# Performance work log

Hardware: AMD Instinct MI355X
Metric: run time of the kernel (lower is better)

## Reference

```python
import jax, jax.numpy as jnp
import numpy as np

WL = 140        # window_length
TD_NUM = 14     # TimeDelayEnd - TimeDelaySta = 21 - 7
OFC = 119       # window_length - TimeDelayEnd
E1 = 119        # td_attn embed dim
E2 = 16         # cm_attn embed dim


def _mha(q, k, v, in_w, in_b, out_w, out_b):
    # single-head MultiheadAttention, torch convention: y = x @ W.T + b
    E = q.shape[-1]
    qp = q @ in_w[:E].T + in_b[:E]
    kp = k @ in_w[E:2 * E].T + in_b[E:2 * E]
    vp = v @ in_w[2 * E:].T + in_b[2 * E:]
    attn = jax.nn.softmax((qp * (E ** -0.5)) @ kp.T, axis=-1)
    return (attn @ vp) @ out_w.T + out_b


def setup_inputs() -> dict:
    key = jax.random.key(0)
    ks = jax.random.split(key, 24)
    n = lambda i, s: jax.random.normal(ks[i], s, dtype=jnp.float32) * 0.05
    return {
        "x": jax.random.normal(ks[0], (1, 1, 18, WL), dtype=jnp.float32),
        "td_in_w": n(1, (3 * E1, E1)), "td_in_b": n(2, (3 * E1,)),
        "td_out_w": n(3, (E1, E1)), "td_out_b": n(4, (E1,)),
        "cm_in_w": n(5, (4, 3 * E2, E2)), "cm_in_b": n(6, (4, 3 * E2)),
        "cm_out_w": n(7, (4, E2, E2)), "cm_out_b": n(8, (4, E2)),
        "mc_w": n(9, (2, 16)), "mc_b": n(10, (2,)),
        "max_fc_w": n(11, (16, 32)), "max_fc_b": n(12, (16,)),
        "proj_w": n(13, (2, 16)),
        "ln_g": jnp.ones((16,), jnp.float32), "ln_b": jnp.zeros((16,), jnp.float32),
        "fc_w": n(14, (2,)), "fc_b": n(15, (2,)),
        "out1_w": n(16, (OFC, 2 * OFC)), "out1_b": n(17, (OFC,)),
        "out2_w": n(18, (2, OFC)), "out2_b": n(19, (2,)),
    }


def reference(x, td_in_w, td_in_b, td_out_w, td_out_b,
              cm_in_w, cm_in_b, cm_out_w, cm_out_b,
              mc_w, mc_b, max_fc_w, max_fc_b, proj_w,
              ln_g, ln_b, fc_w, fc_b, out1_w, out1_b, out2_w, out2_b):
    wavA = x[0, 0, 0]            # [140]
    eeg = x[0, 0, 1:17]          # [16, 140]
    wavB = x[0, 0, 17]           # [140]

    # ChannelWav: vectorized sliding-window gather -> [OFC, TD_NUM]
    idx = jnp.arange(OFC)[:, None] + jnp.arange(TD_NUM)[None, :]
    wA_win = wavA[idx]           # [119, 14]
    wB_win = wavB[idx]

    eeg_q = eeg[:, WL - OFC:]    # [16, 119] (16 eeg channels as seq, embed=119)

    # time-delay attention: query=eeg (len 16), key/value=delayed wav (len 14)
    wA_att = _mha(eeg_q, wA_win.T, wA_win.T, td_in_w, td_in_b, td_out_w, td_out_b)  # [16,119]
    wB_att = _mha(eeg_q, wB_win.T, wB_win.T, td_in_w, td_in_b, td_out_w, td_out_b)

    # select_max: bmm + 1x1 conv + relu + fc + argmax over 16 scores
    vA = jax.nn.relu(mc_w[0] @ (eeg_q @ wA_att.T) + mc_b[0])   # [16]
    vB = jax.nn.relu(mc_w[1] @ (eeg_q @ wB_att.T) + mc_b[1])
    weight = jax.nn.relu(max_fc_w @ jnp.concatenate([vA, vB]) + max_fc_b)
    mi = jnp.argmax(weight)     # note: clamped into [0, TD_NUM) by jnp.take
    wA_sel = jnp.take(wA_win.T, mi, axis=0)   # [119]
    wB_sel = jnp.take(wB_win.T, mi, axis=0)

    # proj_audio: Conv1d(1,16,1,bias=False) == outer product with weight vector
    wA_p = proj_w[0][:, None] * wA_sel[None, :]   # [16,119]
    wB_p = proj_w[1][:, None] * wB_sel[None, :]

    # LayerNorm over the 16-channel axis
    et = eeg_q.T                                   # [119,16]
    mu = et.mean(-1, keepdims=True)
    var = et.var(-1, keepdims=True)
    eeg_ln = (((et - mu) / jnp.sqrt(var + 1e-5)) * ln_g + ln_b).T   # [16,119]

    data = [wA_p, eeg_ln, eeg_ln, wB_p]
    kv = [eeg_ln, wA_p, wB_p, eeg_ln]
    outs = [_mha(data[i].T, kv[i].T, kv[i].T,
                 cm_in_w[i], cm_in_b[i], cm_out_w[i], cm_out_b[i]).T
            for i in range(4)]                      # each [16,119]

    # tensordot + diag == per-position channel dot product
    d0 = jnp.einsum('ct,ct->t', outs[0], outs[1])   # [119]
    d1 = jnp.einsum('ct,ct->t', outs[3], outs[2])
    s0 = jax.nn.sigmoid(fc_w[0] * d0 + fc_b[0])
    s1 = jax.nn.sigmoid(fc_w[1] * d1 + fc_b[1])
    dd = jnp.concatenate([s0, s1])                  # [238]

    h = jax.nn.sigmoid(out1_w @ dd + out1_b)
    return jax.nn.sigmoid(out2_w @ h + out2_b)[None, :]   # [1,2]
```

## Files before the change

kernel.cpp:

```cpp
#include <hip/hip_runtime.h>
#include <math.h>


#define NWG 8
#define NT  1024

constexpr int WLEN = 140;
constexpr int TDN  = 14;
constexpr int NOFC = 119;

constexpr int G_V16 = 0;
constexpr int G_O   = 64;

constexpr int EEG = 0;
constexpr int WA  = 1904;
constexpr int WB  = 2044;
constexpr int LNT = 2184;
constexpr int QP4 = 4088;
constexpr int Z4  = 4564;
constexpr int UD  = 5040;
constexpr int WTT = 5160;
constexpr int WVV = 5280;
constexpr int VT  = 5400;
constexpr int SC4 = 5416;
constexpr int BKQ = 5472;
constexpr int CVB = 5476, CBO = 5477, MIX = 5478;
constexpr int WGT = 5480;
constexpr int WQK = 5500;
constexpr int WEV = 5516;
constexpr int AC  = 5532, BC = 5548;
constexpr int PKQ = 5568;
constexpr int VPS = 7472;
constexpr int S1O = 9852;
constexpr int S2O = 9971;
constexpr int OWS = 10090;
constexpr int OBS = 10346;
constexpr int DD  = 4088;
constexpr int HH  = 4328;
constexpr int ARENA = 10368;

struct Args {
  const float *x, *td_in_w, *td_in_b, *td_out_w, *td_out_b;
  const float *cm_in_w, *cm_in_b, *cm_out_w, *cm_out_b;
  const float *mc_w, *mc_b, *max_fc_w, *max_fc_b, *proj_w;
  const float *ln_g, *ln_b, *fc_w, *fc_b;
  const float *out1_w, *out1_b, *out2_w, *out2_b;
  float *out;
  unsigned int *bar;
  float *G;
};

__device__ __forceinline__ float sigmf(float v) {
  return 1.0f / (1.0f + __expf(-v));
}

__device__ __forceinline__ void gbar(unsigned int* p) {
  __syncthreads();
  if (threadIdx.x == 0) {
    __hip_atomic_fetch_add(p, 1u, __ATOMIC_ACQ_REL, __HIP_MEMORY_SCOPE_AGENT);
    while (__hip_atomic_load(p, __ATOMIC_RELAXED, __HIP_MEMORY_SCOPE_AGENT) < (unsigned)NWG) {
      __builtin_amdgcn_s_sleep(1);
    }
    __builtin_amdgcn_fence(__ATOMIC_ACQUIRE, "agent");
  }
  __syncthreads();
}

__device__ __forceinline__ float dot119(const float* __restrict__ w,
                                        const float* __restrict__ x,
                                        int lane16) {
  float a0 = 0.f, a1 = 0.f;
#pragma unroll
  for (int t = 0; t < 7; ++t) {
    float wv = w[lane16 + 16 * t];
    float xv = x[lane16 + 16 * t];
    if (t & 1) a1 += wv * xv; else a0 += wv * xv;
  }
  if (lane16 < 7) a0 += w[112 + lane16] * x[112 + lane16];
  float acc = a0 + a1;
#pragma unroll
  for (int m = 1; m < 16; m <<= 1) acc += __shfl_xor(acc, m);
  return acc;
}

__device__ __forceinline__ float dot16f4(const float* __restrict__ x,
                                         const float* __restrict__ w) {
  const float4* xa = (const float4*)x; const float4* wa = (const float4*)w;
  float4 x0 = xa[0], x1 = xa[1], x2 = xa[2], x3 = xa[3];
  float4 w0 = wa[0], w1 = wa[1], w2 = wa[2], w3 = wa[3];
  float d0 = x0.x*w0.x + x0.y*w0.y + x0.z*w0.z + x0.w*w0.w;
  float d1 = x1.x*w1.x + x1.y*w1.y + x1.z*w1.z + x1.w*w1.w;
  float d2 = x2.x*w2.x + x2.y*w2.y + x2.z*w2.z + x2.w*w2.w;
  float d3 = x3.x*w3.x + x3.y*w3.y + x3.z*w3.z + x3.w*w3.w;
  return (d0 + d1) + (d2 + d3);
}

__global__ __launch_bounds__(NT) void fused_cnn_kernel(Args a) {
  __shared__ __align__(16) float S[ARENA];
  const int tid = threadIdx.x;
  const int wgid = blockIdx.x;
  const int grp = tid >> 4;
  const int lane16 = tid & 15;
  float* G = a.G;

  const int s  = wgid >> 2;
  const int i0 = (wgid & 3) * 4;
  const int wavs = s ? WB : WA;
  const int m  = (wgid == 2) ? 1 : (wgid == 3) ? 2 : (wgid < 2 || wgid == 6) ? 0 : 3;
  const int r0 = (wgid == 1 || wgid == 5) ? 40 : (wgid >= 6) ? 80 : 0;
  const int nr = (wgid == 2 || wgid == 3) ? 119 : (wgid >= 6) ? 39 : 40;
  const bool heavy = (m == 0) || (m == 3);
  const int pr = (m >= 2) ? 1 : 0;
  const int wavm = (m <= 1) ? WA : WB;

  for (int t = tid; t < 16 * NOFC; t += NT) {
    int c = t / NOFC, tt = t - c * NOFC;
    S[EEG + t] = a.x[(1 + c) * WLEN + (WLEN - NOFC) + tt];
  }
  if (tid < WLEN) {
    S[WA + tid] = a.x[tid];
    S[WB + tid] = a.x[17 * WLEN + tid];
  }
  __syncthreads();

  for (int e = grp; e < NOFC; e += 64) {
    const float* wrow = a.td_in_w + e * NOFC;
    float w0 = wrow[lane16], w1 = wrow[lane16 + 16], w2 = wrow[lane16 + 32],
          w3 = wrow[lane16 + 48], w4 = wrow[lane16 + 64], w5 = wrow[lane16 + 80],
          w6 = wrow[lane16 + 96];
    float wt7 = (lane16 < 7) ? wrow[112 + lane16] : 0.0f;
    float b = a.td_in_b[e];
#pragma unroll
    for (int kk = 0; kk < 4; ++kk) {
      const float* x = S + EEG + (i0 + kk) * NOFC;
      float acc = w0 * x[lane16] + w1 * x[lane16 + 16] + w2 * x[lane16 + 32]
                + w3 * x[lane16 + 48] + w4 * x[lane16 + 64] + w5 * x[lane16 + 80]
                + w6 * x[lane16 + 96];
      if (lane16 < 7) acc += wt7 * x[112 + lane16];
#pragma unroll
      for (int mm = 1; mm < 16; mm <<= 1) acc += __shfl_xor(acc, mm);
      if (lane16 == 0) S[QP4 + kk * NOFC + e] = acc + b;
    }
  }
  __syncthreads();

  if (tid < NOFC) {
    float xv[16]; float mu = 0.f;
#pragma unroll
    for (int c = 0; c < 16; ++c) { xv[c] = S[EEG + c * NOFC + tid]; mu += xv[c]; }
    mu *= (1.0f / 16.0f);
    float var = 0.f;
#pragma unroll
    for (int c = 0; c < 16; ++c) { float d = xv[c] - mu; var += d * d; }
    var *= (1.0f / 16.0f);
    float inv = 1.0f / sqrtf(var + 1e-5f);
#pragma unroll
    for (int c = 0; c < 16; ++c)
      S[LNT + tid * 16 + c] = (xv[c] - mu) * inv * a.ln_g[c] + a.ln_b[c];
  }
  if (tid >= 128 && tid < 128 + NOFC) {
    int d = tid - 128;
    float acc = 0.f;
#pragma unroll
    for (int i = 0; i < 16; ++i) acc += a.mc_w[s * 16 + i] * S[EEG + i * NOFC + d];
    S[UD + d] = acc;
  }
  if (tid >= 256 && tid < 256 + NOFC) {
    int t = tid - 256;
    float a0 = 0.f, a1 = 0.f, a2 = 0.f, a3 = 0.f;
    for (int e = 0; e < NOFC; ++e) {
      float w = a.td_in_w[(NOFC + e) * NOFC + t];
      a0 += S[QP4 + e] * w;
      a1 += S[QP4 + NOFC + e] * w;
      a2 += S[QP4 + 2 * NOFC + e] * w;
      a3 += S[QP4 + 3 * NOFC + e] * w;
    }
    S[Z4 + t] = a0; S[Z4 + NOFC + t] = a1;
    S[Z4 + 2 * NOFC + t] = a2; S[Z4 + 3 * NOFC + t] = a3;
  }
  if (tid >= 384 && tid < 448) {
    int kk = (tid - 384) >> 4;
    float acc = dot119(S + QP4 + kk * NOFC, a.td_in_b + NOFC, lane16);
    if (lane16 == 0) S[BKQ + kk] = acc;
  }
  if (tid >= 512 && tid < 528) {
    int e = tid - 512;
    int row = heavy ? (m * 48 + e) : (m * 48 + 16 + e);
    float acc = 0.f;
#pragma unroll
    for (int c = 0; c < 16; ++c) acc += a.proj_w[pr * 16 + c] * a.cm_in_w[row * 16 + c];
    S[WQK + e] = acc;
  }
  if (!heavy && tid >= 528 && tid < 544) {
    int e = tid - 528;
    float acc = 0.f;
#pragma unroll
    for (int c = 0; c < 16; ++c) acc += a.proj_w[pr * 16 + c] * a.cm_in_w[(m * 48 + 32 + e) * 16 + c];
    S[WEV + e] = acc;
  }
  __syncthreads();

  if (tid < NOFC) {
    float acc = 0.f;
    for (int d = 0; d < NOFC; ++d) acc += S[UD + d] * a.td_out_w[d * NOFC + tid];
    S[WTT + tid] = acc;
  } else if (heavy) {
    for (int o = tid - 128; o < 4080; o += 896) {
      if (o < 1904) {
        int u = o >> 4, e = o & 15;
        S[PKQ + u * 16 + e] = dot16f4(S + LNT + u * 16, a.cm_in_w + (m * 48 + 16 + e) * 16)
                              + a.cm_in_b[m * 48 + 16 + e];
      } else if (o < 3808) {
        int o2 = o - 1904, u = o2 >> 4, e = o2 & 15;
        S[VPS + u * 20 + e] = dot16f4(S + LNT + u * 16, a.cm_in_w + (m * 48 + 32 + e) * 16)
                              + a.cm_in_b[m * 48 + 32 + e];
      } else if (o < 4064) {
        int o2 = o - 3808, c = o2 >> 4, e = o2 & 15;
        S[OWS + e * 16 + c] = a.cm_out_w[m * 256 + o2];
      } else {
        S[OBS + o - 4064] = a.cm_out_b[m * 16 + (o - 4064)];
      }
    }
  } else {
    for (int o = tid - 128; o < 1904; o += 896) {
      int t = o >> 4, e = o & 15;
      S[PKQ + t * 16 + e] = dot16f4(S + LNT + t * 16, a.cm_in_w + (m * 48 + e) * 16)
                            + a.cm_in_b[m * 48 + e];
    }
  }
  __syncthreads();

  if (tid < NOFC) {
    float acc = 0.f;
    for (int e = 0; e < NOFC; ++e) acc += S[WTT + e] * a.td_in_w[(2 * NOFC + e) * NOFC + tid];
    S[WVV + tid] = acc;
  }
  if (grp >= 8 && grp < 64) {
    int idx = grp - 8;
    if (idx < 56) {
      int kk = idx / TDN, j = idx - kk * TDN;
      float acc = dot119(S + wavs + j, S + Z4 + kk * NOFC, lane16);
      if (lane16 == 0)
        S[SC4 + kk * TDN + j] = 0.09166984970282113f * (acc + S[BKQ + kk]);
    }
  }
  __syncthreads();

  if (tid < 4) {
    float* r = S + SC4 + tid * TDN;
    float mx = r[0];
#pragma unroll
    for (int j = 1; j < TDN; ++j) mx = fmaxf(mx, r[j]);
    float sum = 0.f;
#pragma unroll
    for (int j = 0; j < TDN; ++j) { float p = __expf(r[j] - mx); r[j] = p; sum += p; }
    float inv = 1.0f / sum;
#pragma unroll
    for (int j = 0; j < TDN; ++j) r[j] *= inv;
  }
  if (grp >= 1 && grp < 15) {
    int j = grp - 1;
    float acc = dot119(S + wavs + j, S + WVV, lane16);
    if (lane16 == 0) S[VT + j] = acc;
  }
  if (grp == 15) {
    float acc = dot119(a.td_in_b + 2 * NOFC, S + WTT, lane16);
    if (lane16 == 0) S[CVB] = acc;
  }
  if (grp == 16) {
    float acc = dot119(S + UD, a.td_out_b, lane16);
    if (lane16 == 0) S[CBO] = acc;
  }
  if (tid >= 288) {
    if (heavy) {
      int idx = tid - 288;
      if (idx < 238) {
        int u = (idx < NOFC) ? idx : idx - NOFC;
        const float* kpr = S + PKQ + u * 16;
        float acc = 0.f;
        if (idx < NOFC) {
#pragma unroll
          for (int e = 0; e < 16; ++e) acc += S[WQK + e] * kpr[e];
          S[S1O + u] = acc;
        } else {
#pragma unroll
          for (int e = 0; e < 16; ++e) acc += a.cm_in_b[m * 48 + e] * kpr[e];
          S[S2O + u] = acc;
        }
      }
    } else {
      int idx = tid - 288;
      if (idx < NOFC) {
        float acc = 0.f;
#pragma unroll
        for (int e = 0; e < 16; ++e) acc += S[PKQ + idx * 16 + e] * S[WQK + e];
        S[S1O + idx] = acc;
      } else if (idx >= 128 && idx < 144) {
        int c = idx - 128;
        float a1 = 0.f, b1 = 0.f;
#pragma unroll
        for (int e = 0; e < 16; ++e) {
          float ow = a.cm_out_w[m * 256 + c * 16 + e];
          a1 += ow * S[WEV + e];
          b1 += ow * a.cm_in_b[m * 48 + 32 + e];
        }
        S[AC + c] = a1;
        S[BC + c] = b1 + a.cm_out_b[m * 16 + c];
      }
    }
  }
  __syncthreads();

  if (tid < 4) {
    float acc = 0.f;
#pragma unroll
    for (int j = 0; j < TDN; ++j) acc += S[SC4 + tid * TDN + j] * S[VT + j];
    float v = acc + S[CVB] + S[CBO] + a.mc_b[s];
    G[G_V16 + s * 16 + i0 + tid] = fmaxf(v, 0.f);
  }
  gbar(a.bar + 0);

  if (tid < 16) {
    float acc = a.max_fc_b[tid];
#pragma unroll
    for (int c = 0; c < 32; ++c) acc += a.max_fc_w[tid * 32 + c] * G[G_V16 + c];
    S[WGT + tid] = fmaxf(acc, 0.f);
  }
  __syncthreads();
  if (tid == 0) {
    float best = S[WGT]; int mi = 0;
    for (int r = 1; r < 16; ++r) {
      float w = S[WGT + r];
      if (w > best) { best = w; mi = r; }
    }
    if (mi > TDN - 1) mi = TDN - 1;
    S[MIX] = (float)mi;
  }
  __syncthreads();

  {
    const int mi = (int)S[MIX];
    if (heavy) {
      if (grp < nr) {
        const int t = r0 + grp;
        const float wsel = S[wavm + t + mi];
        float p[8];
        float mx = -1e30f;
#pragma unroll
        for (int cc = 0; cc < 8; ++cc) {
          int u = lane16 + cc * 16;
          float sc = (u < NOFC) ? 0.25f * (wsel * S[S1O + u] + S[S2O + u]) : -1e30f;
          p[cc] = sc;
          mx = fmaxf(mx, sc);
        }
#pragma unroll
        for (int d = 1; d < 16; d <<= 1) mx = fmaxf(mx, __shfl_xor(mx, d));
        float sum = 0.f;
#pragma unroll
        for (int cc = 0; cc < 8; ++cc) { p[cc] = __expf(p[cc] - mx); sum += p[cc]; }
#pragma unroll
        for (int d = 1; d < 16; d <<= 1) sum += __shfl_xor(sum, d);
        float inv = 1.0f / sum;

        float oa[16];
#pragma unroll
        for (int e = 0; e < 16; ++e) oa[e] = 0.f;
#pragma unroll
        for (int cc = 0; cc < 8; ++cc) {
          int u = lane16 + cc * 16;
          if (u < NOFC) {
            const float4* v4 = (const float4*)(S + VPS + u * 20);
            float4 v0 = v4[0], v1 = v4[1], v2 = v4[2], v3 = v4[3];
            float pv = p[cc];
            oa[0] += pv*v0.x; oa[1] += pv*v0.y; oa[2] += pv*v0.z; oa[3] += pv*v0.w;
            oa[4] += pv*v1.x; oa[5] += pv*v1.y; oa[6] += pv*v1.z; oa[7] += pv*v1.w;
            oa[8] += pv*v2.x; oa[9] += pv*v2.y; oa[10] += pv*v2.z; oa[11] += pv*v2.w;
            oa[12] += pv*v3.x; oa[13] += pv*v3.y; oa[14] += pv*v3.z; oa[15] += pv*v3.w;
          }
        }
#pragma unroll
        for (int e = 0; e < 16; ++e) {
#pragma unroll
          for (int d = 1; d < 16; d <<= 1) oa[e] += __shfl_xor(oa[e], d);
          oa[e] *= inv;
        }
        float accp = S[OBS + lane16];
#pragma unroll
        for (int e = 0; e < 16; ++e) accp += oa[e] * S[OWS + e * 16 + lane16];
        G[G_O + (m * NOFC + t) * 16 + lane16] = accp;
      }
    } else {
      for (int r = grp; r < NOFC; r += 64) {
        const float gt = S[S1O + r];
        float s0 = 0.f, s1a = 0.f;
#pragma unroll
        for (int cc = 0; cc < 8; ++cc) {
          int u = lane16 + cc * 16;
          if (u < NOFC) {
            float w = S[wavm + u + mi];
            float e1 = __expf(0.25f * gt * w);
            s0 += e1; s1a += e1 * w;
          }
        }
#pragma unroll
        for (int d = 1; d < 16; d <<= 1) {
          s0 += __shfl_xor(s0, d);
          s1a += __shfl_xor(s1a, d);
        }
        float h = s1a / s0;
        G[G_O + (m * NOFC + r) * 16 + lane16] = h * S[AC + lane16] + S[BC + lane16];
      }
    }
  }
  gbar(a.bar + 16);

  if (wgid == 0) {
    for (int o = tid; o < 2 * NOFC; o += NT) {
      int half = o / NOFC, t = o - half * NOFC;
      const float* A = G + G_O + ((half ? 3 : 0) * NOFC + t) * 16;
      const float* B = G + G_O + ((half ? 2 : 1) * NOFC + t) * 16;
      float acc = 0.f;
#pragma unroll
      for (int c = 0; c < 16; ++c) acc += A[c] * B[c];
      S[DD + o] = sigmf(a.fc_w[half] * acc + a.fc_b[half]);
    }
    __syncthreads();
    for (int o = grp; o < NOFC; o += 64) {
      const float* wrow = a.out1_w + o * 238;
      float a0 = 0.f, a1 = 0.f;
#pragma unroll
      for (int t = 0; t < 14; ++t) {
        float wv = wrow[lane16 + 16 * t];
        float xv = S[DD + lane16 + 16 * t];
        if (t & 1) a1 += wv * xv; else a0 += wv * xv;
      }
      if (lane16 < 14) a0 += wrow[224 + lane16] * S[DD + 224 + lane16];
      float acc = a0 + a1;
#pragma unroll
      for (int mm = 1; mm < 16; mm <<= 1) acc += __shfl_xor(acc, mm);
      if (lane16 == 0) S[HH + o] = sigmf(acc + a.out1_b[o]);
    }
    __syncthreads();
    if (tid < 32) {
      int o2 = tid >> 4;
      const float* wrow = a.out2_w + o2 * NOFC;
      float a0 = 0.f;
#pragma unroll
      for (int t = 0; t < 8; ++t) {
        int idx = lane16 + 16 * t;
        if (idx < NOFC) a0 += wrow[idx] * S[HH + idx];
      }
      float acc = a0;
#pragma unroll
      for (int mm = 1; mm < 16; mm <<= 1) acc += __shfl_xor(acc, mm);
      if (lane16 == 0) a.out[o2] = sigmf(acc + a.out2_b[o2]);
    }
  }
}

extern "C" void kernel_launch(void* const* d_in, const int* in_sizes, int n_in,
                              void* d_out, int out_size, void* d_ws, size_t ws_size,
                              hipStream_t stream) {
  Args a;
  a.x        = (const float*)d_in[0];
  a.td_in_w  = (const float*)d_in[1];
  a.td_in_b  = (const float*)d_in[2];
  a.td_out_w = (const float*)d_in[3];
  a.td_out_b = (const float*)d_in[4];
  a.cm_in_w  = (const float*)d_in[5];
  a.cm_in_b  = (const float*)d_in[6];
  a.cm_out_w = (const float*)d_in[7];
  a.cm_out_b = (const float*)d_in[8];
  a.mc_w     = (const float*)d_in[9];
  a.mc_b     = (const float*)d_in[10];
  a.max_fc_w = (const float*)d_in[11];
  a.max_fc_b = (const float*)d_in[12];
  a.proj_w   = (const float*)d_in[13];
  a.ln_g     = (const float*)d_in[14];
  a.ln_b     = (const float*)d_in[15];
  a.fc_w     = (const float*)d_in[16];
  a.fc_b     = (const float*)d_in[17];
  a.out1_w   = (const float*)d_in[18];
  a.out1_b   = (const float*)d_in[19];
  a.out2_w   = (const float*)d_in[20];
  a.out2_b   = (const float*)d_in[21];
  a.out      = (float*)d_out;
  a.bar      = (unsigned int*)d_ws;
  a.G        = (float*)((char*)d_ws + 512);

  hipMemsetAsync(d_ws, 0, 512, stream);
  fused_cnn_kernel<<<dim3(NWG), dim3(NT), 0, stream>>>(a);
}
```

Before: 36.05 us.

## Repartition cross-modal attention per stream and distribute output MLP across workgroups

Each workgroup now owns one stream (A or B) and a 30-row slice, computing the heavy attention and the folded light attention together so that the per-position dot product and sigmoid happen locally. Only the 238 gating values go through global memory instead of four 119x16 output tensors. The final out1/out2 MLP is split across all 8 workgroups, with out1 rows prefetched into LDS, and finished with atomic accumulation plus a last-arriver completion counter. This replaces the serial single-workgroup tail. Several barrier phases are merged, argmax becomes a wave shuffle reduction, and the max-subtraction in softmax is dropped, which risks overflow. The atomic accumulators in the barrier buffer also need to be zeroed before every launch.

```diff
diff --git a/kernel.cpp b/kernel.cpp
--- a/kernel.cpp
+++ b/kernel.cpp
@@ -10,7 +10,7 @@
 constexpr int NOFC = 119;
 
 constexpr int G_V16 = 0;
-constexpr int G_O   = 64;
+constexpr int G_DD  = 64;
 
 constexpr int EEG = 0;
 constexpr int WA  = 1904;
@@ -24,20 +24,33 @@
 constexpr int VT  = 5400;
 constexpr int SC4 = 5416;
 constexpr int BKQ = 5472;
-constexpr int CVB = 5476, CBO = 5477, MIX = 5478;
-constexpr int WGT = 5480;
-constexpr int WQK = 5500;
-constexpr int WEV = 5516;
-constexpr int AC  = 5532, BC = 5548;
-constexpr int PKQ = 5568;
-constexpr int VPS = 7472;
-constexpr int S1O = 9852;
-constexpr int S2O = 9971;
-constexpr int OWS = 10090;
-constexpr int OBS = 10346;
-constexpr int DD  = 4088;
-constexpr int HH  = 4328;
-constexpr int ARENA = 10368;
+constexpr int CVB = 5476, CBO = 5477;
+constexpr int WQH = 5480;
+constexpr int WKL = 5496;
+constexpr int WVL = 5512;
+constexpr int WQT = 5528;
+constexpr int CST = 5544;
+constexpr int AC  = 5548;
+constexpr int BC  = 5564;
+constexpr int G1L = 5580;
+constexpr int MXT = 5612;
+constexpr int MXB = 6124;
+constexpr int KPH = 6144;
+constexpr int VPS = 8048;
+constexpr int S1H = 10428;
+constexpr int S2H = 10547;
+constexpr int OWS = 10668;
+constexpr int OBS = 10924;
+constexpr int O1W = 10944;
+constexpr int O1B = 14544;
+constexpr int O2WS= 14560;
+constexpr int O2B = 14590;
+constexpr int FCW = 14592;
+constexpr int FCB = 14594;
+constexpr int DDL = 14596;
+constexpr int HHL = 14836;
+constexpr int VSL = 14852;
+constexpr int ARENA = 14884;
 
 struct Args {
   const float *x, *td_in_w, *td_in_b, *td_out_w, *td_out_b;
@@ -105,13 +118,12 @@
 
   const int s  = wgid >> 2;
   const int i0 = (wgid & 3) * 4;
-  const int wavs = s ? WB : WA;
-  const int m  = (wgid == 2) ? 1 : (wgid == 3) ? 2 : (wgid < 2 || wgid == 6) ? 0 : 3;
-  const int r0 = (wgid == 1 || wgid == 5) ? 40 : (wgid >= 6) ? 80 : 0;
-  const int nr = (wgid == 2 || wgid == 3) ? 119 : (wgid >= 6) ? 39 : 40;
-  const bool heavy = (m == 0) || (m == 3);
-  const int pr = (m >= 2) ? 1 : 0;
-  const int wavm = (m <= 1) ? WA : WB;
+  const int mh = s ? 3 : 0;
+  const int lm = s ? 2 : 1;
+  const int q4 = wgid & 3;
+  const int r0 = q4 * 30;
+  const int nr = (q4 == 3) ? 29 : 30;
+  const int wavX = s ? WB : WA;
 
   for (int t = tid; t < 16 * NOFC; t += NT) {
     int c = t / NOFC, tt = t - c * NOFC;
@@ -120,6 +132,30 @@
   if (tid < WLEN) {
     S[WA + tid] = a.x[tid];
     S[WB + tid] = a.x[17 * WLEN + tid];
+  }
+  if (tid < 512) {
+    int t16 = tid >> 5, c32 = tid & 31;
+    S[MXT + c32 * 16 + t16] = a.max_fc_w[tid];
+  }
+  if (tid < 16)  S[MXB + tid] = a.max_fc_b[tid];
+  for (int idx = tid; idx < 15 * 238; idx += NT) {
+    int rl = idx / 238, c = idx - rl * 238;
+    int r = wgid * 15 + rl;
+    S[O1W + rl * 240 + c] = (r < NOFC) ? a.out1_w[r * 238 + c] : 0.0f;
+  }
+  if (tid < 15) {
+    int r = wgid * 15 + tid;
+    S[O1B + tid] = (r < NOFC) ? a.out1_b[r] : 0.0f;
+  }
+  if (tid < 30) {
+    int o = tid / 15, j = tid - o * 15;
+    int r = wgid * 15 + j;
+    S[O2WS + tid] = (r < NOFC) ? a.out2_w[o * NOFC + r] : 0.0f;
+  }
+  if (tid < 2) {
+    S[O2B + tid] = a.out2_b[tid];
+    S[FCW + tid] = a.fc_w[tid];
+    S[FCB + tid] = a.fc_b[tid];
   }
   __syncthreads();
 
@@ -142,6 +178,15 @@
       if (lane16 == 0) S[QP4 + kk * NOFC + e] = acc + b;
     }
   }
+  if (grp >= 55) {
+    int d = (grp - 55) * 16 + lane16;
+    if (d < NOFC) {
+      float acc = 0.f;
+#pragma unroll
+      for (int i = 0; i < 16; ++i) acc += a.mc_w[s * 16 + i] * S[EEG + i * NOFC + d];
+      S[UD + d] = acc;
+    }
+  }
   __syncthreads();
 
   if (tid < NOFC) {
@@ -157,16 +202,8 @@
 #pragma unroll
     for (int c = 0; c < 16; ++c)
       S[LNT + tid * 16 + c] = (xv[c] - mu) * inv * a.ln_g[c] + a.ln_b[c];
-  }
-  if (tid >= 128 && tid < 128 + NOFC) {
-    int d = tid - 128;
-    float acc = 0.f;
-#pragma unroll
-    for (int i = 0; i < 16; ++i) acc += a.mc_w[s * 16 + i] * S[EEG + i * NOFC + d];
-    S[UD + d] = acc;
-  }
-  if (tid >= 256 && tid < 256 + NOFC) {
-    int t = tid - 256;
+  } else if (tid >= 128 && tid < 128 + NOFC) {
+    int t = tid - 128;
     float a0 = 0.f, a1 = 0.f, a2 = 0.f, a3 = 0.f;
     for (int e = 0; e < NOFC; ++e) {
       float w = a.td_in_w[(NOFC + e) * NOFC + t];
@@ -177,136 +214,143 @@
     }
     S[Z4 + t] = a0; S[Z4 + NOFC + t] = a1;
     S[Z4 + 2 * NOFC + t] = a2; S[Z4 + 3 * NOFC + t] = a3;
-  }
-  if (tid >= 384 && tid < 448) {
-    int kk = (tid - 384) >> 4;
+  } else if (tid >= 256 && tid < 320) {
+    int kk = (tid - 256) >> 4;
     float acc = dot119(S + QP4 + kk * NOFC, a.td_in_b + NOFC, lane16);
     if (lane16 == 0) S[BKQ + kk] = acc;
-  }
-  if (tid >= 512 && tid < 528) {
-    int e = tid - 512;
-    int row = heavy ? (m * 48 + e) : (m * 48 + 16 + e);
-    float acc = 0.f;
-#pragma unroll
-    for (int c = 0; c < 16; ++c) acc += a.proj_w[pr * 16 + c] * a.cm_in_w[row * 16 + c];
-    S[WQK + e] = acc;
-  }
-  if (!heavy && tid >= 528 && tid < 544) {
-    int e = tid - 528;
-    float acc = 0.f;
-#pragma unroll
-    for (int c = 0; c < 16; ++c) acc += a.proj_w[pr * 16 + c] * a.cm_in_w[(m * 48 + 32 + e) * 16 + c];
-    S[WEV + e] = acc;
+  } else if (tid >= 320 && tid < 320 + NOFC) {
+    int t = tid - 320;
+    float acc = 0.f;
+    for (int d = 0; d < NOFC; ++d) acc += S[UD + d] * a.td_out_w[d * NOFC + t];
+    S[WTT + t] = acc;
+  } else if (tid >= 448 && tid < 464) {
+    int e = tid - 448;
+    float acc = 0.f;
+#pragma unroll
+    for (int c = 0; c < 16; ++c) acc += a.proj_w[s * 16 + c] * a.cm_in_w[(mh * 48 + e) * 16 + c];
+    S[WQH + e] = acc;
+  } else if (tid >= 464 && tid < 480) {
+    int e = tid - 464;
+    float acc = 0.f;
+#pragma unroll
+    for (int c = 0; c < 16; ++c) acc += a.proj_w[s * 16 + c] * a.cm_in_w[(lm * 48 + 16 + e) * 16 + c];
+    S[WKL + e] = acc;
+  } else if (tid >= 480 && tid < 496) {
+    int e = tid - 480;
+    float acc = 0.f;
+#pragma unroll
+    for (int c = 0; c < 16; ++c) acc += a.proj_w[s * 16 + c] * a.cm_in_w[(lm * 48 + 32 + e) * 16 + c];
+    S[WVL + e] = acc;
+  }
+  if (grp >= 36) {
+#pragma unroll
+    for (int rnd = 0; rnd < 2; ++rnd) {
+      int idx = (grp - 36) + rnd * 28;
+      if (idx < 56) {
+        int kk = idx / TDN, j = idx - kk * TDN;
+        float acc = dot119(S + wavX + j, S + Z4 + kk * NOFC, lane16);
+        if (lane16 == 0)
+          S[SC4 + kk * TDN + j] = 0.09166984970282113f * (acc + S[BKQ + kk]);
+      }
+    }
   }
   __syncthreads();
 
   if (tid < NOFC) {
     float acc = 0.f;
-    for (int d = 0; d < NOFC; ++d) acc += S[UD + d] * a.td_out_w[d * NOFC + tid];
-    S[WTT + tid] = acc;
-  } else if (heavy) {
-    for (int o = tid - 128; o < 4080; o += 896) {
+    for (int e = 0; e < NOFC; ++e) acc += S[WTT + e] * a.td_in_w[(2 * NOFC + e) * NOFC + tid];
+    S[WVV + tid] = acc;
+  } else if (tid >= 120 && tid < 124) {
+    int k = tid - 120;
+    float* r = S + SC4 + k * TDN;
+    float mx = r[0];
+#pragma unroll
+    for (int j = 1; j < TDN; ++j) mx = fmaxf(mx, r[j]);
+    float sum = 0.f;
+#pragma unroll
+    for (int j = 0; j < TDN; ++j) { float p = __expf(r[j] - mx); r[j] = p; sum += p; }
+    float inv = 1.0f / sum;
+#pragma unroll
+    for (int j = 0; j < TDN; ++j) r[j] *= inv;
+  } else if (tid >= 128 && tid < 144) {
+    int c = tid - 128;
+    float acc = 0.f;
+#pragma unroll
+    for (int e = 0; e < 16; ++e) acc += a.cm_in_w[(lm * 48 + e) * 16 + c] * S[WKL + e];
+    S[WQT + c] = acc;
+  } else if (tid == 144) {
+    float acc = 0.f;
+#pragma unroll
+    for (int e = 0; e < 16; ++e) acc += a.cm_in_b[lm * 48 + e] * S[WKL + e];
+    S[CST] = acc;
+  } else if (tid >= 160 && tid < 176) {
+    int c = tid - 160;
+    float acc = 0.f;
+#pragma unroll
+    for (int e = 0; e < 16; ++e) acc += a.cm_out_w[lm * 256 + c * 16 + e] * S[WVL + e];
+    S[AC + c] = acc;
+  } else if (tid >= 176 && tid < 192) {
+    int c = tid - 176;
+    float acc = 0.f;
+#pragma unroll
+    for (int e = 0; e < 16; ++e) acc += a.cm_out_w[lm * 256 + c * 16 + e] * a.cm_in_b[lm * 48 + 32 + e];
+    S[BC + c] = acc + a.cm_out_b[lm * 16 + c];
+  } else if (tid == 192) {
+    float acc = 0.f;
+    for (int e = 0; e < NOFC; ++e) acc += a.td_in_b[2 * NOFC + e] * S[WTT + e];
+    S[CVB] = acc;
+  } else if (tid == 193) {
+    float acc = 0.f;
+    for (int d = 0; d < NOFC; ++d) acc += S[UD + d] * a.td_out_b[d];
+    S[CBO] = acc;
+  }
+  if (tid >= 256) {
+    for (int o = tid - 256; o < 4080; o += 768) {
       if (o < 1904) {
         int u = o >> 4, e = o & 15;
-        S[PKQ + u * 16 + e] = dot16f4(S + LNT + u * 16, a.cm_in_w + (m * 48 + 16 + e) * 16)
-                              + a.cm_in_b[m * 48 + 16 + e];
+        S[KPH + o] = dot16f4(S + LNT + u * 16, a.cm_in_w + (mh * 48 + 16 + e) * 16)
+                     + a.cm_in_b[mh * 48 + 16 + e];
       } else if (o < 3808) {
         int o2 = o - 1904, u = o2 >> 4, e = o2 & 15;
-        S[VPS + u * 20 + e] = dot16f4(S + LNT + u * 16, a.cm_in_w + (m * 48 + 32 + e) * 16)
-                              + a.cm_in_b[m * 48 + 32 + e];
+        S[VPS + u * 20 + e] = dot16f4(S + LNT + u * 16, a.cm_in_w + (mh * 48 + 32 + e) * 16)
+                              + a.cm_in_b[mh * 48 + 32 + e];
       } else if (o < 4064) {
         int o2 = o - 3808, c = o2 >> 4, e = o2 & 15;
-        S[OWS + e * 16 + c] = a.cm_out_w[m * 256 + o2];
+        S[OWS + e * 16 + c] = a.cm_out_w[mh * 256 + o2];
       } else {
-        S[OBS + o - 4064] = a.cm_out_b[m * 16 + (o - 4064)];
+        S[OBS + o - 4064] = a.cm_out_b[mh * 16 + (o - 4064)];
       }
     }
-  } else {
-    for (int o = tid - 128; o < 1904; o += 896) {
-      int t = o >> 4, e = o & 15;
-      S[PKQ + t * 16 + e] = dot16f4(S + LNT + t * 16, a.cm_in_w + (m * 48 + e) * 16)
-                            + a.cm_in_b[m * 48 + e];
-    }
-  }
-  __syncthreads();
-
-  if (tid < NOFC) {
-    float acc = 0.f;
-    for (int e = 0; e < NOFC; ++e) acc += S[WTT + e] * a.td_in_w[(2 * NOFC + e) * NOFC + tid];
-    S[WVV + tid] = acc;
-  }
-  if (grp >= 8 && grp < 64) {
-    int idx = grp - 8;
-    if (idx < 56) {
-      int kk = idx / TDN, j = idx - kk * TDN;
-      float acc = dot119(S + wavs + j, S + Z4 + kk * NOFC, lane16);
-      if (lane16 == 0)
-        S[SC4 + kk * TDN + j] = 0.09166984970282113f * (acc + S[BKQ + kk]);
-    }
-  }
-  __syncthreads();
-
-  if (tid < 4) {
-    float* r = S + SC4 + tid * TDN;
-    float mx = r[0];
-#pragma unroll
-    for (int j = 1; j < TDN; ++j) mx = fmaxf(mx, r[j]);
-    float sum = 0.f;
-#pragma unroll
-    for (int j = 0; j < TDN; ++j) { float p = __expf(r[j] - mx); r[j] = p; sum += p; }
-    float inv = 1.0f / sum;
-#pragma unroll
-    for (int j = 0; j < TDN; ++j) r[j] *= inv;
-  }
-  if (grp >= 1 && grp < 15) {
-    int j = grp - 1;
-    float acc = dot119(S + wavs + j, S + WVV, lane16);
-    if (lane16 == 0) S[VT + j] = acc;
-  }
-  if (grp == 15) {
-    float acc = dot119(a.td_in_b + 2 * NOFC, S + WTT, lane16);
-    if (lane16 == 0) S[CVB] = acc;
-  }
-  if (grp == 16) {
-    float acc = dot119(S + UD, a.td_out_b, lane16);
-    if (lane16 == 0) S[CBO] = acc;
-  }
-  if (tid >= 288) {
-    if (heavy) {
-      int idx = tid - 288;
-      if (idx < 238) {
-        int u = (idx < NOFC) ? idx : idx - NOFC;
-        const float* kpr = S + PKQ + u * 16;
-        float acc = 0.f;
-        if (idx < NOFC) {
-#pragma unroll
-          for (int e = 0; e < 16; ++e) acc += S[WQK + e] * kpr[e];
-          S[S1O + u] = acc;
-        } else {
-#pragma unroll
-          for (int e = 0; e < 16; ++e) acc += a.cm_in_b[m * 48 + e] * kpr[e];
-          S[S2O + u] = acc;
-        }
-      }
+  }
+  __syncthreads();
+
+  if (grp < TDN) {
+    float acc = dot119(S + wavX + grp, S + WVV, lane16);
+    if (lane16 == 0) S[VT + grp] = acc;
+  }
+  if (tid >= 256 && tid < 256 + 30) {
+    int rl = tid - 256;
+    if (rl < nr) {
+      int t = r0 + rl;
+      float acc = S[CST];
+#pragma unroll
+      for (int c = 0; c < 16; ++c) acc += S[LNT + t * 16 + c] * S[WQT + c];
+      S[G1L + rl] = acc;
+    }
+  }
+  if (tid >= 512 && tid < 512 + 238) {
+    int idx = tid - 512;
+    int u = (idx < NOFC) ? idx : idx - NOFC;
+    const float* kpr = S + KPH + u * 16;
+    float acc = 0.f;
+    if (idx < NOFC) {
+#pragma unroll
+      for (int e = 0; e < 16; ++e) acc += S[WQH + e] * kpr[e];
+      S[S1H + u] = acc;
     } else {
-      int idx = tid - 288;
-      if (idx < NOFC) {
-        float acc = 0.f;
-#pragma unroll
-        for (int e = 0; e < 16; ++e) acc += S[PKQ + idx * 16 + e] * S[WQK + e];
-        S[S1O + idx] = acc;
-      } else if (idx >= 128 && idx < 144) {
-        int c = idx - 128;
-        float a1 = 0.f, b1 = 0.f;
-#pragma unroll
-        for (int e = 0; e < 16; ++e) {
-          float ow = a.cm_out_w[m * 256 + c * 16 + e];
-          a1 += ow * S[WEV + e];
-          b1 += ow * a.cm_in_b[m * 48 + 32 + e];
-        }
-        S[AC + c] = a1;
-        S[BC + c] = b1 + a.cm_out_b[m * 16 + c];
-      }
+#pragma unroll
+      for (int e = 0; e < 16; ++e) acc += a.cm_in_b[mh * 48 + e] * kpr[e];
+      S[S2H + u] = acc;
     }
   }
   __syncthreads();
@@ -320,140 +364,129 @@
   }
   gbar(a.bar + 0);
 
-  if (tid < 16) {
-    float acc = a.max_fc_b[tid];
-#pragma unroll
-    for (int c = 0; c < 32; ++c) acc += a.max_fc_w[tid * 32 + c] * G[G_V16 + c];
-    S[WGT + tid] = fmaxf(acc, 0.f);
+  if (tid < 32) S[VSL + tid] = G[G_V16 + tid];
+  __syncthreads();
+  int mi;
+  {
+    float wl = S[MXB + lane16];
+#pragma unroll
+    for (int c = 0; c < 32; ++c) wl += S[MXT + c * 16 + lane16] * S[VSL + c];
+    wl = fmaxf(wl, 0.f);
+    float mx = wl;
+#pragma unroll
+    for (int d = 1; d < 16; d <<= 1) mx = fmaxf(mx, __shfl_xor(mx, d));
+    int cand = (wl == mx) ? lane16 : 99;
+#pragma unroll
+    for (int d = 1; d < 16; d <<= 1) cand = min(cand, __shfl_xor(cand, d));
+    mi = min(cand, TDN - 1);
+  }
+
+  if (grp < nr) {
+    const int t = r0 + grp;
+    const float wselq = S[wavX + t + mi];
+    float p[8];
+    float sum = 0.f;
+#pragma unroll
+    for (int cc = 0; cc < 8; ++cc) {
+      int u = lane16 + cc * 16;
+      float e1 = 0.f;
+      if (u < NOFC)
+        e1 = __expf(0.25f * (wselq * S[S1H + u] + S[S2H + u]));
+      p[cc] = e1;
+      sum += e1;
+    }
+#pragma unroll
+    for (int d = 1; d < 16; d <<= 1) sum += __shfl_xor(sum, d);
+    float inv = 1.0f / sum;
+
+    float oa[16];
+#pragma unroll
+    for (int e = 0; e < 16; ++e) oa[e] = 0.f;
+#pragma unroll
+    for (int cc = 0; cc < 8; ++cc) {
+      int u = lane16 + cc * 16;
+      if (u < NOFC) {
+        const float4* v4 = (const float4*)(S + VPS + u * 20);
+        float4 v0 = v4[0], v1 = v4[1], v2 = v4[2], v3 = v4[3];
+        float pv = p[cc];
+        oa[0] += pv*v0.x; oa[1] += pv*v0.y; oa[2] += pv*v0.z; oa[3] += pv*v0.w;
+        oa[4] += pv*v1.x; oa[5] += pv*v1.y; oa[6] += pv*v1.z; oa[7] += pv*v1.w;
+        oa[8] += pv*v2.x; oa[9] += pv*v2.y; oa[10] += pv*v2.z; oa[11] += pv*v2.w;
+        oa[12] += pv*v3.x; oa[13] += pv*v3.y; oa[14] += pv*v3.z; oa[15] += pv*v3.w;
+      }
+    }
+#pragma unroll
+    for (int e = 0; e < 16; ++e) {
+#pragma unroll
+      for (int d = 1; d < 16; d <<= 1) oa[e] += __shfl_xor(oa[e], d);
+    }
+    float oc = S[OBS + lane16];
+#pragma unroll
+    for (int e = 0; e < 16; ++e) oc += oa[e] * inv * S[OWS + e * 16 + lane16];
+    float dA = oc * S[AC + lane16];
+    float dB = oc * S[BC + lane16];
+#pragma unroll
+    for (int d = 1; d < 16; d <<= 1) {
+      dA += __shfl_xor(dA, d);
+      dB += __shfl_xor(dB, d);
+    }
+    const float g = S[G1L + grp];
+    float s0 = 0.f, s1a = 0.f;
+#pragma unroll
+    for (int cc = 0; cc < 8; ++cc) {
+      int u = lane16 + cc * 16;
+      if (u < NOFC) {
+        float w = S[wavX + u + mi];
+        float e1 = __expf(0.25f * g * w);
+        s0 += e1; s1a += e1 * w;
+      }
+    }
+#pragma unroll
+    for (int d = 1; d < 16; d <<= 1) {
+      s0 += __shfl_xor(s0, d);
+      s1a += __shfl_xor(s1a, d);
+    }
+    float h = s1a / s0;
+    float dval = h * dA + dB;
+    if (lane16 == 0)
+      G[G_DD + s * NOFC + t] = sigmf(S[FCW + s] * dval + S[FCB + s]);
+  }
+  gbar(a.bar + 16);
+
+  if (tid < 238) S[DDL + tid] = G[G_DD + tid];
+  __syncthreads();
+  if (grp < 15) {
+    int r = wgid * 15 + grp;
+    float acc = 0.f;
+#pragma unroll
+    for (int k = 0; k < 15; ++k) {
+      int c = lane16 + 16 * k;
+      if (c < 238) acc += S[O1W + grp * 240 + c] * S[DDL + c];
+    }
+#pragma unroll
+    for (int d = 1; d < 16; d <<= 1) acc += __shfl_xor(acc, d);
+    if (lane16 == 0)
+      S[HHL + grp] = (r < NOFC) ? sigmf(acc + S[O1B + grp]) : 0.0f;
   }
   __syncthreads();
   if (tid == 0) {
-    float best = S[WGT]; int mi = 0;
-    for (int r = 1; r < 16; ++r) {
-      float w = S[WGT + r];
-      if (w > best) { best = w; mi = r; }
-    }
-    if (mi > TDN - 1) mi = TDN - 1;
-    S[MIX] = (float)mi;
-  }
-  __syncthreads();
-
-  {
-    const int mi = (int)S[MIX];
-    if (heavy) {
-      if (grp < nr) {
-        const int t = r0 + grp;
-        const float wsel = S[wavm + t + mi];
-        float p[8];
-        float mx = -1e30f;
-#pragma unroll
-        for (int cc = 0; cc < 8; ++cc) {
-          int u = lane16 + cc * 16;
-          float sc = (u < NOFC) ? 0.25f * (wsel * S[S1O + u] + S[S2O + u]) : -1e30f;
-          p[cc] = sc;
-          mx = fmaxf(mx, sc);
-        }
-#pragma unroll
-        for (int d = 1; d < 16; d <<= 1) mx = fmaxf(mx, __shfl_xor(mx, d));
-        float sum = 0.f;
-#pragma unroll
-        for (int cc = 0; cc < 8; ++cc) { p[cc] = __expf(p[cc] - mx); sum += p[cc]; }
-#pragma unroll
-        for (int d = 1; d < 16; d <<= 1) sum += __shfl_xor(sum, d);
-        float inv = 1.0f / sum;
-
-        float oa[16];
-#pragma unroll
-        for (int e = 0; e < 16; ++e) oa[e] = 0.f;
-#pragma unroll
-        for (int cc = 0; cc < 8; ++cc) {
-          int u = lane16 + cc * 16;
-          if (u < NOFC) {
-            const float4* v4 = (const float4*)(S + VPS + u * 20);
-            float4 v0 = v4[0], v1 = v4[1], v2 = v4[2], v3 = v4[3];
-            float pv = p[cc];
-            oa[0] += pv*v0.x; oa[1] += pv*v0.y; oa[2] += pv*v0.z; oa[3] += pv*v0.w;
-            oa[4] += pv*v1.x; oa[5] += pv*v1.y; oa[6] += pv*v1.z; oa[7] += pv*v1.w;
-            oa[8] += pv*v2.x; oa[9] += pv*v2.y; oa[10] += pv*v2.z; oa[11] += pv*v2.w;
-            oa[12] += pv*v3.x; oa[13] += pv*v3.y; oa[14] += pv*v3.z; oa[15] += pv*v3.w;
-          }
-        }
-#pragma unroll
-        for (int e = 0; e < 16; ++e) {
-#pragma unroll
-          for (int d = 1; d < 16; d <<= 1) oa[e] += __shfl_xor(oa[e], d);
-          oa[e] *= inv;
-        }
-        float accp = S[OBS + lane16];
-#pragma unroll
-        for (int e = 0; e < 16; ++e) accp += oa[e] * S[OWS + e * 16 + lane16];
-        G[G_O + (m * NOFC + t) * 16 + lane16] = accp;
-      }
-    } else {
-      for (int r = grp; r < NOFC; r += 64) {
-        const float gt = S[S1O + r];
-        float s0 = 0.f, s1a = 0.f;
-#pragma unroll
-        for (int cc = 0; cc < 8; ++cc) {
-          int u = lane16 + cc * 16;
-          if (u < NOFC) {
-            float w = S[wavm + u + mi];
-            float e1 = __expf(0.25f * gt * w);
-            s0 += e1; s1a += e1 * w;
-          }
-        }
-#pragma unroll
-        for (int d = 1; d < 16; d <<= 1) {
-          s0 += __shfl_xor(s0, d);
-          s1a += __shfl_xor(s1a, d);
-        }
-        float h = s1a / s0;
-        G[G_O + (m * NOFC + r) * 16 + lane16] = h * S[AC + lane16] + S[BC + lane16];
-      }
-    }
-  }
-  gbar(a.bar + 16);
-
-  if (wgid == 0) {
-    for (int o = tid; o < 2 * NOFC; o += NT) {
-      int half = o / NOFC, t = o - half * NOFC;
-      const float* A = G + G_O + ((half ? 3 : 0) * NOFC + t) * 16;
-      const float* B = G + G_O + ((half ? 2 : 1) * NOFC + t) * 16;
-      float acc = 0.f;
-#pragma unroll
-      for (int c = 0; c < 16; ++c) acc += A[c] * B[c];
-      S[DD + o] = sigmf(a.fc_w[half] * acc + a.fc_b[half]);
-    }
-    __syncthreads();
-    for (int o = grp; o < NOFC; o += 64) {
-      const float* wrow = a.out1_w + o * 238;
-      float a0 = 0.f, a1 = 0.f;
-#pragma unroll
-      for (int t = 0; t < 14; ++t) {
-        float wv = wrow[lane16 + 16 * t];
-        float xv = S[DD + lane16 + 16 * t];
-        if (t & 1) a1 += wv * xv; else a0 += wv * xv;
-      }
-      if (lane16 < 14) a0 += wrow[224 + lane16] * S[DD + 224 + lane16];
-      float acc = a0 + a1;
-#pragma unroll
-      for (int mm = 1; mm < 16; mm <<= 1) acc += __shfl_xor(acc, mm);
-      if (lane16 == 0) S[HH + o] = sigmf(acc + a.out1_b[o]);
-    }
-    __syncthreads();
-    if (tid < 32) {
-      int o2 = tid >> 4;
-      const float* wrow = a.out2_w + o2 * NOFC;
-      float a0 = 0.f;
-#pragma unroll
-      for (int t = 0; t < 8; ++t) {
-        int idx = lane16 + 16 * t;
-        if (idx < NOFC) a0 += wrow[idx] * S[HH + idx];
-      }
-      float acc = a0;
-#pragma unroll
-      for (int mm = 1; mm < 16; mm <<= 1) acc += __shfl_xor(acc, mm);
-      if (lane16 == 0) a.out[o2] = sigmf(acc + a.out2_b[o2]);
+    float p0 = 0.f, p1 = 0.f;
+#pragma unroll
+    for (int j = 0; j < 15; ++j) {
+      p0 += S[O2WS + j] * S[HHL + j];
+      p1 += S[O2WS + 15 + j] * S[HHL + j];
+    }
+    float* acc = (float*)((char*)a.bar + 128);
+    unsigned int* done = (unsigned int*)((char*)a.bar + 192);
+    __hip_atomic_fetch_add(acc + 0, p0, __ATOMIC_RELAXED, __HIP_MEMORY_SCOPE_AGENT);
+    __hip_atomic_fetch_add(acc + 1, p1, __ATOMIC_RELAXED, __HIP_MEMORY_SCOPE_AGENT);
+    unsigned old = __hip_atomic_fetch_add(done, 1u, __ATOMIC_ACQ_REL, __HIP_MEMORY_SCOPE_AGENT);
+    if (old == NWG - 1) {
+      __builtin_amdgcn_fence(__ATOMIC_ACQUIRE, "agent");
+      float a0 = __hip_atomic_load(acc + 0, __ATOMIC_RELAXED, __HIP_MEMORY_SCOPE_AGENT);
+      float a1 = __hip_atomic_load(acc + 1, __ATOMIC_RELAXED, __HIP_MEMORY_SCOPE_AGENT);
+      a.out[0] = sigmf(a0 + S[O2B + 0]);
+      a.out[1] = sigmf(a1 + S[O2B + 1]);
     }
   }
 }
```

Result: faster. 34.66 us (-3.8%).
